# Kernel optimization log

Hardware: AMD Instinct MI355X
Metric: run time of the kernel (lower is better)

## Reference

```python
import jax, jax.numpy as jnp
import numpy as np
import math

TANH_CLIP = 10.0
MAX_TIME = 1440.0


def setup_inputs() -> dict:
    key = jax.random.key(0)
    ks = jax.random.split(key, 16)
    B, N, D, S = 1024, 512, 128, 3
    sc = 1.0 / math.sqrt(D)
    inp = {
        'node_emb': jax.random.normal(ks[0], (B, N, D), jnp.float32),
        'W_last': jax.random.normal(ks[1], (D, D), jnp.float32) * sc,
        'W_first': jax.random.normal(ks[2], (D, D), jnp.float32) * sc,
        'W_graph': jax.random.normal(ks[3], (D, D), jnp.float32) * sc,
        'W_visited': jax.random.normal(ks[4], (D, D), jnp.float32) * sc,
        'W_key': jax.random.normal(ks[5], (D, D), jnp.float32) * sc,
        'W_state': jax.random.normal(ks[6], (S, D), jnp.float32) * sc,
        'b_state': jnp.zeros((D,), jnp.float32),
        'current_time': jax.random.uniform(ks[7], (B, 1), jnp.float32) * MAX_TIME,
        'used_capacity': jax.random.uniform(ks[8], (B, 1), jnp.float32),
        'vehicle_capacity': jnp.ones((B, 1), jnp.float32),
        'travel_time_matrix': jax.random.uniform(ks[9], (N, N), jnp.float32) * MAX_TIME,
        'current_node': jax.random.randint(ks[10], (B, 1), 0, N, jnp.int32),
        'previous_action': jax.random.randint(ks[11], (B, 1), 0, N, jnp.int32),
        'first_node': jax.random.randint(ks[12], (B,), 0, N, jnp.int32),
        'visited': jax.random.randint(ks[13], (B, N), 0, 2, jnp.int32).astype(bool),
        'action_mask': jax.random.randint(ks[14], (B, N), 0, 2, jnp.int32).astype(bool),
        'i': jax.random.randint(ks[15], (B, 1), 0, 2 * N, jnp.int32),
        'h3_indices': jax.random.randint(jax.random.fold_in(key, 99), (B, N), 0, N, jnp.int32),
    }
    return inp


def reference(node_emb, W_last, W_first, W_graph, W_visited, W_key, W_state, b_state,
              current_time, used_capacity, vehicle_capacity, travel_time_matrix,
              current_node, previous_action, first_node, visited, action_mask, i, h3_indices):
    B, N, D = node_emb.shape
    barange = jnp.arange(B)

    # precompute (cache)
    K = jnp.einsum('bnd,de->bne', node_emb, W_key)          # [B,N,D]
    graph_emb = node_emb.mean(axis=1)                        # [B,D]

    # first-node bookkeeping
    cur = current_node[:, 0]
    prev = previous_action[:, 0]
    left_depot = (prev == 0) & (cur != 0)
    fn = jnp.where(left_depot, cur, first_node)
    fn = jnp.where(cur == 0, jnp.zeros_like(fn), fn)

    # context gathers
    h_current = node_emb[barange, cur]                       # [B,D]
    h_first = node_emb[barange, fn]                          # [B,D]
    vf = visited.astype(node_emb.dtype)                      # [B,N]
    vcount = jnp.clip(vf.sum(axis=-1, keepdims=True), 1.0)
    h_visited = jnp.einsum('bn,bnd->bd', vf, node_emb) / vcount

    # scalar state features
    remaining_cap = (vehicle_capacity - used_capacity)[:, 0]
    ct = current_time[:, 0] / MAX_TIME
    step_feat = i[:, 0].astype(node_emb.dtype) / (N * 2)
    state_feats = jnp.stack([remaining_cap, ct, step_feat], axis=-1)  # [B,3]

    q = (h_current @ W_last + h_first @ W_first + graph_emb @ W_graph
         + h_visited @ W_visited + state_feats @ W_state + b_state)   # [B,D]

    score = jnp.einsum('bd,bnd->bn', q, K) / math.sqrt(D)   # [B,N]

    # travel-time bias (shared 2D matrix)
    cur_h3 = h3_indices[barange, cur]                        # [B]
    row = travel_time_matrix[cur_h3]                         # [B,N]
    travel = jnp.take_along_axis(row, h3_indices, axis=1)    # [B,N]
    score = score - travel / MAX_TIME / math.sqrt(2.0)

    score = TANH_CLIP * jnp.tanh(score / TANH_CLIP)
    score = jnp.where(action_mask, score, -1e8)
    return jax.nn.log_softmax(score, axis=-1)
```

## Files before the change

kernel.cpp:

```cpp
#include <hip/hip_runtime.h>
#include <math.h>

#define NB 1024
#define NN 512
#define ND 128
#define NT 512
#define DYN_BYTES (NN * ND)

typedef float f4 __attribute__((ext_vector_type(4)));

__device__ __forceinline__ f4 ldnt(const float* p) {
    return __builtin_nontemporal_load(reinterpret_cast<const f4*>(p));
}

#define QSC   15.875f
#define DQSC  (8.0f / 127.0f)

__global__ __launch_bounds__(NT, 4) void darp_fused(
    const float* __restrict__ node_emb,
    const float* __restrict__ W_last,
    const float* __restrict__ W_first,
    const float* __restrict__ W_graph,
    const float* __restrict__ W_visited,
    const float* __restrict__ W_key,
    const float* __restrict__ W_state,
    const float* __restrict__ b_state,
    const float* __restrict__ current_time,
    const float* __restrict__ used_capacity,
    const float* __restrict__ vehicle_capacity,
    const float* __restrict__ ttm,
    const int* __restrict__ current_node,
    const int* __restrict__ previous_action,
    const int* __restrict__ first_node,
    const int* __restrict__ visited,
    const int* __restrict__ action_mask,
    const int* __restrict__ step_i,
    const int* __restrict__ h3_indices,
    float* __restrict__ out)
{
    const int b    = blockIdx.x;
    const int t    = threadIdx.x;
    const int wave = t >> 6;
    const int lane = t & 63;
    const int l5   = t & 31;
    const int strm = t >> 5;

    __shared__ float4 sgh[8][32];
    __shared__ float4 svh[8][32];
    __shared__ unsigned long long smask[8];
    __shared__ float  smean[ND];
    __shared__ float  svis[ND];
    __shared__ float  shcur[ND];
    __shared__ float  shfirst[ND];
    __shared__ float  qs[ND];
    __shared__ float  qp[ND];
    __shared__ float  scratch[512];
    __shared__ float  sred[16];
    __shared__ float  s_scal[4];
    extern __shared__ signed char tile[];

    {
        const int f = (visited[(size_t)b * NN + t] != 0);
        unsigned long long m = __ballot(f);
        if (lane == 0) smask[wave] = m;
        float vc = f ? 1.0f : 0.0f;
#pragma unroll
        for (int off = 32; off >= 1; off >>= 1) vc += __shfl_xor(vc, off);
        if (lane == 0) sred[wave] = vc;
    }
    __syncthreads();

    const float* nbp = node_emb + (size_t)b * NN * ND;

    {
        const int r0 = strm * 32;
        const float* p = nbp + (size_t)r0 * ND + l5 * 4;
        const unsigned int mybits =
            (unsigned int)(smask[strm >> 1] >> ((strm & 1) * 32));
        unsigned int* tl = reinterpret_cast<unsigned int*>(tile) + r0 * 32 + l5;

        float4 g = make_float4(0.f, 0.f, 0.f, 0.f);
        float4 v = make_float4(0.f, 0.f, 0.f, 0.f);

        f4 xa[8], xb[8];
#pragma unroll
        for (int u = 0; u < 8; ++u) xa[u] = ldnt(p + (size_t)u * ND);
#pragma unroll
        for (int u = 0; u < 8; ++u) xb[u] = ldnt(p + (size_t)(8 + u) * ND);

#define PROC8(BUF, BASE)                                                       \
        {                                                                      \
            _Pragma("unroll")                                                  \
            for (int u = 0; u < 8; ++u) {                                      \
                const f4 X = BUF[u];                                           \
                const int k = (BASE) + u;                                      \
                const float vf = ((mybits >> k) & 1u) ? 1.0f : 0.0f;           \
                g.x += X.x; g.y += X.y; g.z += X.z; g.w += X.w;                \
                v.x = fmaf(vf, X.x, v.x); v.y = fmaf(vf, X.y, v.y);            \
                v.z = fmaf(vf, X.z, v.z); v.w = fmaf(vf, X.w, v.w);            \
                const int i0 = __float2int_rn(fminf(fmaxf(X.x * QSC, -127.f), 127.f)); \
                const int i1 = __float2int_rn(fminf(fmaxf(X.y * QSC, -127.f), 127.f)); \
                const int i2 = __float2int_rn(fminf(fmaxf(X.z * QSC, -127.f), 127.f)); \
                const int i3 = __float2int_rn(fminf(fmaxf(X.w * QSC, -127.f), 127.f)); \
                const unsigned int w = (unsigned int)(i0 & 255)                \
                    | ((unsigned int)(i1 & 255) << 8)                          \
                    | ((unsigned int)(i2 & 255) << 16)                         \
                    | ((unsigned int)(i3 & 255) << 24);                        \
                tl[k * 32] = w;                                                \
            }                                                                  \
        }

        PROC8(xa, 0)
#pragma unroll
        for (int u = 0; u < 8; ++u) xa[u] = ldnt(p + (size_t)(16 + u) * ND);
        PROC8(xb, 8)
#pragma unroll
        for (int u = 0; u < 8; ++u) xb[u] = ldnt(p + (size_t)(24 + u) * ND);
        PROC8(xa, 16)
        PROC8(xb, 24)
#undef PROC8

        g.x += __shfl_xor(g.x, 32); g.y += __shfl_xor(g.y, 32);
        g.z += __shfl_xor(g.z, 32); g.w += __shfl_xor(g.w, 32);
        v.x += __shfl_xor(v.x, 32); v.y += __shfl_xor(v.y, 32);
        v.z += __shfl_xor(v.z, 32); v.w += __shfl_xor(v.w, 32);
        if (lane < 32) { sgh[wave][l5] = g; svh[wave][l5] = v; }
    }
    __syncthreads();

    int cur  = current_node[b];
    int prev = previous_action[b];
    int fn   = first_node[b];
    if (prev == 0 && cur != 0) fn = cur;
    if (cur == 0) fn = 0;

    if (t < ND) {
        shcur[t]   = nbp[(size_t)cur * ND + t];
        shfirst[t] = nbp[(size_t)fn  * ND + t];
    }
    if (t < 32) {
        float4 G = sgh[0][t], V = svh[0][t];
#pragma unroll
        for (int j = 1; j < 8; ++j) {
            float4 a = sgh[j][t], d = svh[j][t];
            G.x += a.x; G.y += a.y; G.z += a.z; G.w += a.w;
            V.x += d.x; V.y += d.y; V.z += d.z; V.w += d.w;
        }
        const float invN = 1.0f / (float)NN;
        smean[t * 4 + 0] = G.x * invN; smean[t * 4 + 1] = G.y * invN;
        smean[t * 4 + 2] = G.z * invN; smean[t * 4 + 3] = G.w * invN;
        svis[t * 4 + 0] = V.x; svis[t * 4 + 1] = V.y;
        svis[t * 4 + 2] = V.z; svis[t * 4 + 3] = V.w;
    }
    if (t == 0) {
        float c = sred[0] + sred[1] + sred[2] + sred[3]
                + sred[4] + sred[5] + sred[6] + sred[7];
        s_scal[0] = 1.0f / fmaxf(c, 1.0f);
        s_scal[1] = vehicle_capacity[b] - used_capacity[b];
        s_scal[2] = current_time[b] * (1.0f / 1440.0f);
        s_scal[3] = (float)step_i[b] * (1.0f / (2.0f * (float)NN));
    }
    __syncthreads();

    {
        const int e  = t & 127;
        const int g2 = t >> 7;
        const int d0 = g2 * 32;
        float a0 = 0.f, a1 = 0.f, a2 = 0.f, a3 = 0.f;
#pragma unroll 8
        for (int dd = 0; dd < 32; ++dd) {
            int d = d0 + dd;
            a0 = fmaf(shcur[d],   W_last[d * ND + e],    a0);
            a1 = fmaf(shfirst[d], W_first[d * ND + e],   a1);
            a2 = fmaf(smean[d],   W_graph[d * ND + e],   a2);
            a3 = fmaf(svis[d],    W_visited[d * ND + e], a3);
        }
        float pacc = a0 + a1 + a2 + s_scal[0] * a3;
        if (g2 == 0) {
            pacc += b_state[e]
                  + s_scal[1] * W_state[e]
                  + s_scal[2] * W_state[ND + e]
                  + s_scal[3] * W_state[2 * ND + e];
        }
        scratch[g2 * 128 + e] = pacc;
    }
    __syncthreads();

    if (t < ND) qs[t] = scratch[t] + scratch[128 + t]
                      + scratch[256 + t] + scratch[384 + t];
    __syncthreads();

    {
        float4 qv = *reinterpret_cast<const float4*>(&qs[l5 * 4]);
#pragma unroll
        for (int it = 0; it < 8; ++it) {
            int d = it * 16 + strm;
            float4 wk = *reinterpret_cast<const float4*>(W_key + (size_t)d * ND + l5 * 4);
            float s = wk.x * qv.x + wk.y * qv.y + wk.z * qv.z + wk.w * qv.w;
            s += __shfl_xor(s, 16); s += __shfl_xor(s, 8);
            s += __shfl_xor(s, 4);  s += __shfl_xor(s, 2); s += __shfl_xor(s, 1);
            if (l5 == 0) qp[d] = s * (0.08838834764831845f * DQSC);
        }
    }
    __syncthreads();

    {
        const float4 qv = *reinterpret_cast<const float4*>(&qp[l5 * 4]);
        const unsigned int* tu = reinterpret_cast<const unsigned int*>(tile);
        const int n0 = strm * 32;
#pragma unroll 4
        for (int it = 0; it < 32; ++it) {
            const int n = n0 + it;
            const unsigned int w = tu[n * 32 + l5];
            const float f0 = (float)((int)(w << 24) >> 24);
            const float f1 = (float)((int)(w << 16) >> 24);
            const float f2 = (float)((int)(w <<  8) >> 24);
            const float f3 = (float)((int)w >> 24);
            float s = f0 * qv.x + f1 * qv.y + f2 * qv.z + f3 * qv.w;
            s += __shfl_xor(s, 16); s += __shfl_xor(s, 8);
            s += __shfl_xor(s, 4);  s += __shfl_xor(s, 2); s += __shfl_xor(s, 1);
            if (l5 == 0) scratch[n] = s;
        }
    }
    __syncthreads();

    {
        const int    cur_h3 = h3_indices[(size_t)b * NN + cur];
        const float* trow   = ttm + (size_t)cur_h3 * NN;
        const float  tscale = 1.0f / (1440.0f * 1.4142135623730951f);

        float s1 = scratch[t];
        int   h1 = h3_indices[(size_t)b * NN + t];
        s1 -= trow[h1] * tscale;
        s1 = 10.0f * tanhf(s1 * 0.1f);
        if (!action_mask[(size_t)b * NN + t]) s1 = -1e8f;

        float m = s1;
#pragma unroll
        for (int off = 32; off >= 1; off >>= 1) m = fmaxf(m, __shfl_xor(m, off));
        if (lane == 0) sred[wave] = m;
        __syncthreads();
        float bm = fmaxf(fmaxf(fmaxf(sred[0], sred[1]), fmaxf(sred[2], sred[3])),
                         fmaxf(fmaxf(sred[4], sred[5]), fmaxf(sred[6], sred[7])));

        float es = expf(s1 - bm);
#pragma unroll
        for (int off = 32; off >= 1; off >>= 1) es += __shfl_xor(es, off);
        if (lane == 0) sred[8 + wave] = es;
        __syncthreads();
        float lse = bm + logf(sred[8]  + sred[9]  + sred[10] + sred[11]
                            + sred[12] + sred[13] + sred[14] + sred[15]);

        out[(size_t)b * NN + t] = s1 - lse;
    }
}

extern "C" void kernel_launch(void* const* d_in, const int* in_sizes, int n_in,
                              void* d_out, int out_size, void* d_ws, size_t ws_size,
                              hipStream_t stream) {
    (void)in_sizes; (void)n_in; (void)d_ws; (void)ws_size; (void)out_size;
    hipFuncSetAttribute(reinterpret_cast<const void*>(darp_fused),
                        hipFuncAttributeMaxDynamicSharedMemorySize, DYN_BYTES);
    darp_fused<<<dim3(NB), dim3(NT), DYN_BYTES, stream>>>(
        (const float*)d_in[0],
        (const float*)d_in[1],
        (const float*)d_in[2],
        (const float*)d_in[3],
        (const float*)d_in[4],
        (const float*)d_in[5],
        (const float*)d_in[6],
        (const float*)d_in[7],
        (const float*)d_in[8],
        (const float*)d_in[9],
        (const float*)d_in[10],
        (const float*)d_in[11],
        (const int*)d_in[12],
        (const int*)d_in[13],
        (const int*)d_in[14],
        (const int*)d_in[15],
        (const int*)d_in[16],
        (const int*)d_in[17],
        (const int*)d_in[18],
        (float*)d_out);
}
```

Measured before the change: 86.42 us.

## XOR-swizzle int8 tile so each thread computes one node score without shuffles

Writes the quantized embedding tile with an XOR swizzle, which lets each thread read a full node row without LDS bank conflicts. Each thread then computes its own node's score with FMAs, replacing the 32-lane shuffle reductions, the scratch round-trip and one barrier. Static shared memory now replaces the dynamic allocation, with sgh/svh aliased onto scratch. The loads of the current and first node rows are moved before the main streaming loop so their latency is hidden. The cost is more LDS reads of qp per thread and a heavier per-thread dot-product loop.

```diff
diff --git a/kernel.cpp b/kernel.cpp
--- a/kernel.cpp
+++ b/kernel.cpp
@@ -5,7 +5,6 @@
 #define NN 512
 #define ND 128
 #define NT 512
-#define DYN_BYTES (NN * ND)
 
 typedef float f4 __attribute__((ext_vector_type(4)));
 
@@ -45,19 +44,33 @@
     const int l5   = t & 31;
     const int strm = t >> 5;
 
-    __shared__ float4 sgh[8][32];
-    __shared__ float4 svh[8][32];
+    __shared__ char  smem_u[8192] __attribute__((aligned(16)));
     __shared__ unsigned long long smask[8];
-    __shared__ float  smean[ND];
-    __shared__ float  svis[ND];
-    __shared__ float  shcur[ND];
-    __shared__ float  shfirst[ND];
-    __shared__ float  qs[ND];
-    __shared__ float  qp[ND];
-    __shared__ float  scratch[512];
-    __shared__ float  sred[16];
-    __shared__ float  s_scal[4];
-    extern __shared__ signed char tile[];
+    __shared__ float smean[ND];
+    __shared__ float svis[ND];
+    __shared__ float shcur[ND];
+    __shared__ float shfirst[ND];
+    __shared__ float qs[ND];
+    __shared__ float qp[ND] __attribute__((aligned(16)));
+    __shared__ float sred[16];
+    __shared__ float s_scal[4];
+    __shared__ unsigned int tile[NN * 32];
+
+    float4 (*sgh)[32] = reinterpret_cast<float4(*)[32]>(smem_u);
+    float4 (*svh)[32] = reinterpret_cast<float4(*)[32]>(smem_u + 4096);
+    float*  scratch   = reinterpret_cast<float*>(smem_u);
+
+    const float* nbp = node_emb + (size_t)b * NN * ND;
+
+    int cur  = current_node[b];
+    int prev = previous_action[b];
+    int fn   = first_node[b];
+    if (prev == 0 && cur != 0) fn = cur;
+    if (cur == 0) fn = 0;
+
+    float4 hc4, hf4;
+    if (t < 32)       hc4 = *reinterpret_cast<const float4*>(nbp + (size_t)cur * ND + t * 4);
+    else if (t < 64)  hf4 = *reinterpret_cast<const float4*>(nbp + (size_t)fn  * ND + (t - 32) * 4);
 
     {
         const int f = (visited[(size_t)b * NN + t] != 0);
@@ -70,14 +83,12 @@
     }
     __syncthreads();
 
-    const float* nbp = node_emb + (size_t)b * NN * ND;
-
     {
         const int r0 = strm * 32;
         const float* p = nbp + (size_t)r0 * ND + l5 * 4;
         const unsigned int mybits =
             (unsigned int)(smask[strm >> 1] >> ((strm & 1) * 32));
-        unsigned int* tl = reinterpret_cast<unsigned int*>(tile) + r0 * 32 + l5;
+        unsigned int* tw = tile + r0 * 32;
 
         float4 g = make_float4(0.f, 0.f, 0.f, 0.f);
         float4 v = make_float4(0.f, 0.f, 0.f, 0.f);
@@ -106,7 +117,7 @@
                     | ((unsigned int)(i1 & 255) << 8)                          \
                     | ((unsigned int)(i2 & 255) << 16)                         \
                     | ((unsigned int)(i3 & 255) << 24);                        \
-                tl[k * 32] = w;                                                \
+                tw[k * 32 + (l5 ^ k)] = w;                                     \
             }                                                                  \
         }
 
@@ -128,31 +139,25 @@
     }
     __syncthreads();
 
-    int cur  = current_node[b];
-    int prev = previous_action[b];
-    int fn   = first_node[b];
-    if (prev == 0 && cur != 0) fn = cur;
-    if (cur == 0) fn = 0;
-
-    if (t < ND) {
-        shcur[t]   = nbp[(size_t)cur * ND + t];
-        shfirst[t] = nbp[(size_t)fn  * ND + t];
-    }
-    if (t < 32) {
-        float4 G = sgh[0][t], V = svh[0][t];
+    if (t < 32)       *reinterpret_cast<float4*>(&shcur[t * 4]) = hc4;
+    else if (t < 64)  *reinterpret_cast<float4*>(&shfirst[(t - 32) * 4]) = hf4;
+
+    if (t >= 64 && t < 96) {
+        const int c = t - 64;
+        float4 G = sgh[0][c], V = svh[0][c];
 #pragma unroll
         for (int j = 1; j < 8; ++j) {
-            float4 a = sgh[j][t], d = svh[j][t];
+            float4 a = sgh[j][c], d = svh[j][c];
             G.x += a.x; G.y += a.y; G.z += a.z; G.w += a.w;
             V.x += d.x; V.y += d.y; V.z += d.z; V.w += d.w;
         }
         const float invN = 1.0f / (float)NN;
-        smean[t * 4 + 0] = G.x * invN; smean[t * 4 + 1] = G.y * invN;
-        smean[t * 4 + 2] = G.z * invN; smean[t * 4 + 3] = G.w * invN;
-        svis[t * 4 + 0] = V.x; svis[t * 4 + 1] = V.y;
-        svis[t * 4 + 2] = V.z; svis[t * 4 + 3] = V.w;
-    }
-    if (t == 0) {
+        smean[c * 4 + 0] = G.x * invN; smean[c * 4 + 1] = G.y * invN;
+        smean[c * 4 + 2] = G.z * invN; smean[c * 4 + 3] = G.w * invN;
+        svis[c * 4 + 0] = V.x; svis[c * 4 + 1] = V.y;
+        svis[c * 4 + 2] = V.z; svis[c * 4 + 3] = V.w;
+    }
+    if (t == 128) {
         float c = sred[0] + sred[1] + sred[2] + sred[3]
                 + sred[4] + sred[5] + sred[6] + sred[7];
         s_scal[0] = 1.0f / fmaxf(c, 1.0f);
@@ -205,32 +210,26 @@
     __syncthreads();
 
     {
-        const float4 qv = *reinterpret_cast<const float4*>(&qp[l5 * 4]);
-        const unsigned int* tu = reinterpret_cast<const unsigned int*>(tile);
-        const int n0 = strm * 32;
-#pragma unroll 4
-        for (int it = 0; it < 32; ++it) {
-            const int n = n0 + it;
-            const unsigned int w = tu[n * 32 + l5];
+        const unsigned int* tr = tile + t * 32;
+        const int sw = t & 31;
+        float s1 = 0.f;
+#pragma unroll 8
+        for (int c = 0; c < 32; ++c) {
+            const unsigned int w = tr[c ^ sw];
+            const float4 q4 = *reinterpret_cast<const float4*>(&qp[c * 4]);
             const float f0 = (float)((int)(w << 24) >> 24);
             const float f1 = (float)((int)(w << 16) >> 24);
             const float f2 = (float)((int)(w <<  8) >> 24);
             const float f3 = (float)((int)w >> 24);
-            float s = f0 * qv.x + f1 * qv.y + f2 * qv.z + f3 * qv.w;
-            s += __shfl_xor(s, 16); s += __shfl_xor(s, 8);
-            s += __shfl_xor(s, 4);  s += __shfl_xor(s, 2); s += __shfl_xor(s, 1);
-            if (l5 == 0) scratch[n] = s;
-        }
-    }
-    __syncthreads();
-
-    {
+            s1 = fmaf(f0, q4.x, s1); s1 = fmaf(f1, q4.y, s1);
+            s1 = fmaf(f2, q4.z, s1); s1 = fmaf(f3, q4.w, s1);
+        }
+
         const int    cur_h3 = h3_indices[(size_t)b * NN + cur];
         const float* trow   = ttm + (size_t)cur_h3 * NN;
         const float  tscale = 1.0f / (1440.0f * 1.4142135623730951f);
 
-        float s1 = scratch[t];
-        int   h1 = h3_indices[(size_t)b * NN + t];
+        int h1 = h3_indices[(size_t)b * NN + t];
         s1 -= trow[h1] * tscale;
         s1 = 10.0f * tanhf(s1 * 0.1f);
         if (!action_mask[(size_t)b * NN + t]) s1 = -1e8f;
@@ -259,9 +258,7 @@
                               void* d_out, int out_size, void* d_ws, size_t ws_size,
                               hipStream_t stream) {
     (void)in_sizes; (void)n_in; (void)d_ws; (void)ws_size; (void)out_size;
-    hipFuncSetAttribute(reinterpret_cast<const void*>(darp_fused),
-                        hipFuncAttributeMaxDynamicSharedMemorySize, DYN_BYTES);
-    darp_fused<<<dim3(NB), dim3(NT), DYN_BYTES, stream>>>(
+    darp_fused<<<dim3(NB), dim3(NT), 0, stream>>>(
         (const float*)d_in[0],
         (const float*)d_in[1],
         (const float*)d_in[2],
```

Result: no change. 87.58 us (+1.3%).
